# Kernel tuning notes

Measured on AMD Instinct MI355X. Metric: run time of the kernel, lower is better.

The kernel has to match this reference:

```python
import jax, jax.numpy as jnp
import numpy as np

B, S, D = 32, 577, 768
H, Dh = 12, 64  # num_attention_heads, attention_head_size = pruned_dim // heads


def setup_inputs() -> dict:
    key = jax.random.key(0)
    ks = jax.random.split(key, 7)
    s = 1.0 / np.sqrt(D)
    return {
        "hidden_states": jax.random.normal(ks[0], (B, S, D), dtype=jnp.float32),
        "Wq": jax.random.normal(ks[1], (D, H * Dh), dtype=jnp.float32) * s,
        "bq": jnp.zeros((H * Dh,), dtype=jnp.float32),
        "Wk": jax.random.normal(ks[2], (D, H * Dh), dtype=jnp.float32) * s,
        "bk": jnp.zeros((H * Dh,), dtype=jnp.float32),
        "Wv": jax.random.normal(ks[3], (D, H * Dh), dtype=jnp.float32) * s,
        "bv": jnp.zeros((H * Dh,), dtype=jnp.float32),
    }


def reference(hidden_states, Wq, bq, Wk, bk, Wv, bv):
    def heads(x):  # [B,S,H*Dh] -> [B,H,S,Dh]
        return x.reshape(B, S, H, Dh).transpose(0, 2, 1, 3)

    q = heads(hidden_states @ Wq + bq)
    k = heads(hidden_states @ Wk + bk)
    v = heads(hidden_states @ Wv + bv)

    scale = 1.0 / np.sqrt(Dh)
    scores = jnp.einsum("bhqd,bhkd->bhqk", q, k) * scale  # [B,H,S,S]
    probs = jax.nn.softmax(scores, axis=-1)  # dropout p=0.0 -> identity
    ctx = jnp.einsum("bhqk,bhkd->bhqd", probs, v)  # [B,H,S,Dh]
    ctx = ctx.transpose(0, 2, 1, 3).reshape(B, S, H * Dh)
    return ctx
```

## Files before the change

kernel.cpp:

```cpp
#include <hip/hip_runtime.h>

#define NB 32
#define SEQ 577
#define SP 640
#define DM 768
#define NH 12
#define DH 64
#define NC 10

typedef __attribute__((ext_vector_type(8))) short bf16x8;
typedef __attribute__((ext_vector_type(4))) short bf16x4;
typedef __attribute__((ext_vector_type(4))) float f32x4;
typedef __attribute__((ext_vector_type(2))) unsigned int u32x2;
typedef __attribute__((ext_vector_type(4))) unsigned int u32x4;
typedef unsigned short u16;

__device__ __forceinline__ u16 f2bf(float f) {
  unsigned int u = __builtin_bit_cast(unsigned int, f);
  u += 0x7fffu + ((u >> 16) & 1u);
  return (u16)(u >> 16);
}

__device__ __forceinline__ unsigned int pack_bf2(float a, float b) {
  unsigned int ua = __builtin_bit_cast(unsigned int, a) + 0x8000u;
  unsigned int ub = __builtin_bit_cast(unsigned int, b) + 0x8000u;
  return __builtin_amdgcn_perm(ub, ua, 0x07060302u);
}

__device__ __forceinline__ void g2l16(const void* g, void* lds) {
  __builtin_amdgcn_global_load_lds(
      (const __attribute__((address_space(1))) void*)g,
      (__attribute__((address_space(3))) void*)lds, 16, 0, 0);
}

__global__ void cvt_x_kernel(const float* __restrict__ X, u16* __restrict__ Xb, int n4) {
  int i = blockIdx.x * 256 + threadIdx.x;
  if (i >= n4) return;
  f32x4 v = *reinterpret_cast<const f32x4*>(X + (size_t)i * 4);
  u32x2 p;
  p[0] = (unsigned)f2bf(v[0]) | ((unsigned)f2bf(v[1]) << 16);
  p[1] = (unsigned)f2bf(v[2]) | ((unsigned)f2bf(v[3]) << 16);
  *reinterpret_cast<u32x2*>(Xb + (size_t)i * 4) = p;
}

__global__ __launch_bounds__(256)
void cvt_w_kernel(const float* __restrict__ Wq, const float* __restrict__ Wk,
                  const float* __restrict__ Wv, u16* __restrict__ Wt) {
  __shared__ u16 ld[64 * 72];
  const int m = blockIdx.z;
  const float* W = (m == 0) ? Wq : (m == 1) ? Wk : Wv;
  const int k0 = blockIdx.y * 64, n0 = blockIdx.x * 64;
  const int tid = threadIdx.x;
  const int kr = tid >> 4, c4 = tid & 15;
#pragma unroll
  for (int p = 0; p < 4; ++p) {
    const int k = p * 16 + kr;
    f32x4 v = *reinterpret_cast<const f32x4*>(&W[(size_t)(k0 + k) * DM + n0 + c4 * 4]);
#pragma unroll
    for (int e = 0; e < 4; ++e) ld[(c4 * 4 + e) * 72 + k] = f2bf(v[e]);
  }
  __syncthreads();
  u16* dst = Wt + (size_t)m * DM * DM;
#pragma unroll
  for (int p = 0; p < 2; ++p) {
    const int s = p * 256 + tid;
    const int n = s >> 3, ch = (s & 7) * 8;
    u32x4 w = *reinterpret_cast<const u32x4*>(&ld[n * 72 + ch]);
    *reinterpret_cast<u32x4*>(&dst[(size_t)(n0 + n) * DM + k0 + ch]) = w;
  }
}

__global__ __launch_bounds__(512, 2)
void qkv_gemm_kernel(const u16* __restrict__ Xb, const u16* __restrict__ Wt,
                     const float* __restrict__ bq, const float* __restrict__ bk,
                     const float* __restrict__ bv,
                     u16* __restrict__ Qw, u16* __restrict__ Kw, u16* __restrict__ Vw,
                     const int qkv) {
  __shared__ alignas(16) u16 sh[256 * 264];

  const int tid = threadIdx.x;
  const int lane = tid & 63;
  const int wid = tid >> 6;
  const int wm = wid >> 2, wn = wid & 3;
  const int l15 = lane & 15, lq = lane >> 4;

  const int flat = blockIdx.y * 80 + blockIdx.x;
  const int xcd = flat & 7;
  const int j8 = flat >> 3;
  const int xi = j8 / 3;
  const int nt = j8 - xi * 3;
  const int mt = xi * 8 + xcd;

  const u16* Wm = Wt + (size_t)qkv * DM * DM;
  const float* bias = (qkv == 0) ? bq : (qkv == 1) ? bk : bv;

  const u16* gA[2];
  const u16* gB[2];
#pragma unroll
  for (int s = 0; s < 2; ++s) {
    const int e = wid * 2 + s;
    int r = mt * 256 + e * 16 + l15;
    int br = r / SP;
    int tr = r - br * SP;
    if (tr >= SEQ) tr = SEQ - 1;
    gA[s] = Xb + (size_t)(br * SEQ + tr) * DM + lq * 8;
    gB[s] = Wm + (size_t)(nt * 256 + e * 16 + l15) * DM + lq * 8;
  }

  f32x4 acc[8][4];
#pragma unroll
  for (int i = 0; i < 8; ++i)
#pragma unroll
    for (int j = 0; j < 4; ++j)
#pragma unroll
      for (int r = 0; r < 4; ++r) acc[i][j][r] = 0.0f;

  auto stageA = [&](int buf, int kt) {
    g2l16(gA[0] + kt * 32, &sh[buf * 8192 + (wid * 2 + 0) * 512]);
    g2l16(gA[1] + kt * 32, &sh[buf * 8192 + (wid * 2 + 1) * 512]);
  };
  auto stageB = [&](int buf, int kt) {
    g2l16(gB[0] + kt * 32, &sh[32768 + buf * 8192 + (wid * 2 + 0) * 512]);
    g2l16(gB[1] + kt * 32, &sh[32768 + buf * 8192 + (wid * 2 + 1) * 512]);
  };

  stageA(0, 0); stageB(0, 0);
  stageA(1, 1); stageB(1, 1);
  stageA(2, 2); stageB(2, 2);
  asm volatile("s_waitcnt vmcnt(8)" ::: "memory");
  __builtin_amdgcn_s_barrier();

  const int NKT = DM / 32;
  for (int kt = 0; kt < NKT; ++kt) {
    const int buf = kt & 3;
    const int nbuf = (kt + 3) & 3;
    const bool more = (kt + 3 < NKT);
    bf16x8 a03[4], bf4[4], a47[4];

#pragma unroll
    for (int i = 0; i < 4; ++i)
      a03[i] = *reinterpret_cast<const bf16x8*>(&sh[buf * 8192 + ((wm * 8 + i) * 64 + lane) * 8]);
#pragma unroll
    for (int j = 0; j < 4; ++j)
      bf4[j] = *reinterpret_cast<const bf16x8*>(&sh[32768 + buf * 8192 + ((wn * 4 + j) * 64 + lane) * 8]);
    if (more) stageA(nbuf, kt + 3);
    __builtin_amdgcn_s_barrier();
    __builtin_amdgcn_s_setprio(1);
#pragma unroll
    for (int i = 0; i < 4; ++i)
#pragma unroll
      for (int j = 0; j < 4; ++j)
        acc[i][j] = __builtin_amdgcn_mfma_f32_16x16x32_bf16(a03[i], bf4[j], acc[i][j], 0, 0, 0);
    __builtin_amdgcn_s_setprio(0);
    __builtin_amdgcn_s_barrier();

#pragma unroll
    for (int i = 0; i < 4; ++i)
      a47[i] = *reinterpret_cast<const bf16x8*>(&sh[buf * 8192 + ((wm * 8 + 4 + i) * 64 + lane) * 8]);
    if (more) stageB(nbuf, kt + 3);
    if (kt <= NKT - 4) {
      asm volatile("s_waitcnt vmcnt(8)" ::: "memory");
    } else if (kt == NKT - 3) {
      asm volatile("s_waitcnt vmcnt(4)" ::: "memory");
    } else if (kt == NKT - 2) {
      asm volatile("s_waitcnt vmcnt(0)" ::: "memory");
    }
    __builtin_amdgcn_s_barrier();
    __builtin_amdgcn_s_setprio(1);
#pragma unroll
    for (int i = 0; i < 4; ++i)
#pragma unroll
      for (int j = 0; j < 4; ++j)
        acc[4 + i][j] = __builtin_amdgcn_mfma_f32_16x16x32_bf16(a47[i], bf4[j], acc[4 + i][j], 0, 0, 0);
    __builtin_amdgcn_s_setprio(0);
    __builtin_amdgcn_s_barrier();
  }

  const float sfold = 0.18033688011112042f;
#pragma unroll
  for (int j = 0; j < 4; ++j) {
    const int col = wn * 64 + j * 16 + l15;
    const float bb = bias[nt * 256 + col];
#pragma unroll
    for (int i = 0; i < 8; ++i) {
      const int row = wm * 128 + i * 16 + lq * 4;
      if (qkv == 2) {
        unsigned p0 = (unsigned)f2bf(acc[i][j][0] + bb) | ((unsigned)f2bf(acc[i][j][1] + bb) << 16);
        unsigned p1 = (unsigned)f2bf(acc[i][j][2] + bb) | ((unsigned)f2bf(acc[i][j][3] + bb) << 16);
        *reinterpret_cast<u32x2*>(&sh[col * 264 + row]) = u32x2{p0, p1};
      } else {
#pragma unroll
        for (int r = 0; r < 4; ++r) {
          float v = acc[i][j][r] + bb;
          if (qkv == 0) v *= sfold;
          sh[(row + r) * 264 + col] = f2bf(v);
        }
      }
    }
  }
  __builtin_amdgcn_s_barrier();

#pragma unroll
  for (int p = 0; p < 16; ++p) {
    const int slot = p * 512 + tid;
    const int rr = slot >> 5;
    const int cc = (slot & 31) * 8;
    u32x4 w = *reinterpret_cast<const u32x4*>(&sh[rr * 264 + cc]);
    if (qkv == 2) {
      const int gcol = nt * 256 + rr;
      const int h = gcol >> 6, d = gcol & 63;
      const int rg = mt * 256 + cc;
      const int br = rg / SP, tr = rg - br * SP;
      *reinterpret_cast<u32x4*>(&Vw[((size_t)(br * NH + h) * DH + d) * SP + tr]) = w;
    } else {
      const int rg = mt * 256 + rr;
      const int br = rg / SP, tr = rg - br * SP;
      const int gcol = nt * 256 + cc;
      const int h = gcol >> 6, d = gcol & 63;
      u16* dst = ((qkv == 0) ? Qw : Kw) + ((size_t)(br * NH + h) * SP + tr) * DH + d;
      *reinterpret_cast<u32x4*>(dst) = w;
    }
  }
}

#if __has_builtin(__builtin_amdgcn_mfma_f32_16x16x16bf16_1k)
#define MFMA16(a, b, c) __builtin_amdgcn_mfma_f32_16x16x16bf16_1k(a, b, c, 0, 0, 0)
#define HAVE_MFMA16 1
#elif __has_builtin(__builtin_amdgcn_mfma_f32_16x16x16_bf16)
#define MFMA16(a, b, c) __builtin_amdgcn_mfma_f32_16x16x16_bf16(a, b, c, 0, 0, 0)
#define HAVE_MFMA16 1
#else
#define HAVE_MFMA16 0
#endif

__global__ __launch_bounds__(256)
void attn_kernel(const u16* __restrict__ Qw, const u16* __restrict__ Kw,
                 const u16* __restrict__ Vw, float* __restrict__ out) {
  __shared__ alignas(16) u16 Kc[2][8 * 64 * 8];
  __shared__ alignas(16) u16 Vc[2][16 * 64 * 4];

  const int tid = threadIdx.x;
  const int lane = tid & 63;
  const int wid = tid >> 6;
  const int l15 = lane & 15, lq = lane >> 4;

  const int flat = blockIdx.y * 5 + blockIdx.x;
  const int w = (flat & 7) * 240 + (flat >> 3);
  const int qx = w % 5;
  const int bh = w / 5;
  const int b = bh / NH;
  const int h = bh - b * NH;
  const int q0 = qx * 128 + wid * 32;

  const u16* Qb = Qw + (size_t)bh * SP * DH;
  const u16* Kb = Kw + (size_t)bh * SP * DH;
  const u16* Vb = Vw + (size_t)bh * DH * SP;

  bf16x8 qf[2][2];
#pragma unroll
  for (int qt = 0; qt < 2; ++qt)
#pragma unroll
    for (int hf = 0; hf < 2; ++hf)
      qf[qt][hf] = *reinterpret_cast<const bf16x8*>(
          &Qb[(q0 + qt * 16 + l15) * DH + hf * 32 + lq * 8]);

  const u16* gK = Kb + (size_t)(wid * 16 + l15) * DH + lq * 8;
  const u16* gV = Vb + (size_t)(wid * 16 + l15) * SP + lq * 4;

  float mrow[2] = {-__builtin_inff(), -__builtin_inff()};
  float lrow[2] = {0.0f, 0.0f};
  f32x4 acc[2][4];
#pragma unroll
  for (int qt = 0; qt < 2; ++qt)
#pragma unroll
    for (int dt = 0; dt < 4; ++dt)
#pragma unroll
      for (int r = 0; r < 4; ++r) acc[qt][dt][r] = 0.0f;

  g2l16(gK, &Kc[0][(wid * 2 + 0) * 512]);
  g2l16(gK + 32, &Kc[0][(wid * 2 + 1) * 512]);
  {
    u32x2 v[4];
#pragma unroll
    for (int t = 0; t < 4; ++t)
      v[t] = *reinterpret_cast<const u32x2*>(gV + t * 16);
#pragma unroll
    for (int t = 0; t < 4; ++t)
      *reinterpret_cast<u32x2*>(&Vc[0][((wid * 4 + t) * 64 + lane) * 4]) = v[t];
  }
  __syncthreads();

  for (int c = 0; c < NC; ++c) {
    const int cur = c & 1;
    const int c0 = c * 64;
    u32x2 vn[4];
    if (c + 1 < NC) {
      const u16* gKn = gK + (size_t)(c0 + 64) * DH;
      g2l16(gKn, &Kc[cur ^ 1][(wid * 2 + 0) * 512]);
      g2l16(gKn + 32, &Kc[cur ^ 1][(wid * 2 + 1) * 512]);
#pragma unroll
      for (int t = 0; t < 4; ++t)
        vn[t] = *reinterpret_cast<const u32x2*>(gV + (c0 + 64) + t * 16);
    }

    f32x4 s[2][4];
    __builtin_amdgcn_s_setprio(1);
#pragma unroll
    for (int t = 0; t < 4; ++t) {
      bf16x8 kf0 = *reinterpret_cast<const bf16x8*>(&Kc[cur][((t * 2 + 0) * 64 + lane) * 8]);
      bf16x8 kf1 = *reinterpret_cast<const bf16x8*>(&Kc[cur][((t * 2 + 1) * 64 + lane) * 8]);
#pragma unroll
      for (int qt = 0; qt < 2; ++qt) {
        f32x4 z;
#pragma unroll
        for (int r = 0; r < 4; ++r) z[r] = 0.0f;
        z = __builtin_amdgcn_mfma_f32_16x16x32_bf16(kf0, qf[qt][0], z, 0, 0, 0);
        z = __builtin_amdgcn_mfma_f32_16x16x32_bf16(kf1, qf[qt][1], z, 0, 0, 0);
        s[qt][t] = z;
      }
    }
    __builtin_amdgcn_s_setprio(0);
    if (c0 + 64 > SEQ) {
#pragma unroll
      for (int qt = 0; qt < 2; ++qt)
#pragma unroll
        for (int t = 0; t < 4; ++t)
#pragma unroll
          for (int r = 0; r < 4; ++r) {
            int key = c0 + t * 16 + lq * 4 + r;
            s[qt][t][r] = (key < SEQ) ? s[qt][t][r] : -__builtin_inff();
          }
    }
    float alpha[2];
    unsigned int pku[2][4][2];
#pragma unroll
    for (int qt = 0; qt < 2; ++qt) {
      float mx = s[qt][0][0];
#pragma unroll
      for (int t = 0; t < 4; ++t)
#pragma unroll
        for (int r = 0; r < 4; ++r) mx = fmaxf(mx, s[qt][t][r]);
      mx = fmaxf(mx, __shfl_xor(mx, 16));
      mx = fmaxf(mx, __shfl_xor(mx, 32));
      float mn = fmaxf(mrow[qt], mx);
      alpha[qt] = __builtin_amdgcn_exp2f(mrow[qt] - mn);
      mrow[qt] = mn;
      float sm = 0.0f;
#pragma unroll
      for (int t = 0; t < 4; ++t) {
        float p0 = __builtin_amdgcn_exp2f(s[qt][t][0] - mn);
        float p1 = __builtin_amdgcn_exp2f(s[qt][t][1] - mn);
        float p2 = __builtin_amdgcn_exp2f(s[qt][t][2] - mn);
        float p3 = __builtin_amdgcn_exp2f(s[qt][t][3] - mn);
        sm += (p0 + p1) + (p2 + p3);
        pku[qt][t][0] = pack_bf2(p0, p1);
        pku[qt][t][1] = pack_bf2(p2, p3);
      }
      sm += __shfl_xor(sm, 16);
      sm += __shfl_xor(sm, 32);
      lrow[qt] = lrow[qt] * alpha[qt] + sm;
    }

#if HAVE_MFMA16
    __builtin_amdgcn_s_setprio(1);
#pragma unroll
    for (int dt = 0; dt < 4; ++dt) {
      bf16x4 vf[4];
#pragma unroll
      for (int t = 0; t < 4; ++t)
        vf[t] = *reinterpret_cast<const bf16x4*>(&Vc[cur][((dt * 4 + t) * 64 + lane) * 4]);
#pragma unroll
      for (int qt = 0; qt < 2; ++qt) {
        f32x4 a = acc[qt][dt];
#pragma unroll
        for (int r = 0; r < 4; ++r) a[r] *= alpha[qt];
#pragma unroll
        for (int t = 0; t < 4; ++t) {
          bf16x4 pf = __builtin_bit_cast(bf16x4, u32x2{pku[qt][t][0], pku[qt][t][1]});
          a = MFMA16(vf[t], pf, a);
        }
        acc[qt][dt] = a;
      }
    }
    __builtin_amdgcn_s_setprio(0);
#else
#pragma unroll
    for (int qt = 0; qt < 2; ++qt) {
      unsigned int bfrag[2][4];
#pragma unroll
      for (int hh = 0; hh < 2; ++hh)
#pragma unroll
        for (int w2 = 0; w2 < 4; ++w2) {
          int srcl = l15 + 16 * (2 * (lq & 1) + (w2 >> 1));
          unsigned int lo = (unsigned int)__shfl((int)pku[qt][2 * hh][w2 & 1], srcl);
          unsigned int hi = (unsigned int)__shfl((int)pku[qt][2 * hh + 1][w2 & 1], srcl);
          bfrag[hh][w2] = (lq < 2) ? lo : hi;
        }
#pragma unroll
      for (int dt = 0; dt < 4; ++dt) {
        f32x4 a = acc[qt][dt];
#pragma unroll
        for (int r = 0; r < 4; ++r) a[r] *= alpha[qt];
#pragma unroll
        for (int hh = 0; hh < 2; ++hh) {
          u32x2 w0 = *reinterpret_cast<const u32x2*>(&Vc[cur][((dt * 4 + 2 * hh) * 64 + lane) * 4]);
          u32x2 w1 = *reinterpret_cast<const u32x2*>(&Vc[cur][((dt * 4 + 2 * hh + 1) * 64 + lane) * 4]);
          u32x4 vw = {w0[0], w0[1], w1[0], w1[1]};
          u32x4 pw = {bfrag[hh][0], bfrag[hh][1], bfrag[hh][2], bfrag[hh][3]};
          a = __builtin_amdgcn_mfma_f32_16x16x32_bf16(
              __builtin_bit_cast(bf16x8, vw), __builtin_bit_cast(bf16x8, pw), a, 0, 0, 0);
        }
        acc[qt][dt] = a;
      }
    }
#endif

    if (c + 1 < NC) {
#pragma unroll
      for (int t = 0; t < 4; ++t)
        *reinterpret_cast<u32x2*>(&Vc[cur ^ 1][((wid * 4 + t) * 64 + lane) * 4]) = vn[t];
    }
    __syncthreads();
  }

#pragma unroll
  for (int qt = 0; qt < 2; ++qt) {
    int q = q0 + qt * 16 + l15;
    if (q < SEQ) {
      float rl = 1.0f / lrow[qt];
      float* orow = out + ((size_t)b * SEQ + q) * DM + h * DH;
#pragma unroll
      for (int dt = 0; dt < 4; ++dt) {
        f32x4 v = acc[qt][dt];
#pragma unroll
        for (int r = 0; r < 4; ++r) v[r] *= rl;
        *reinterpret_cast<f32x4*>(&orow[dt * 16 + lq * 4]) = v;
      }
    }
  }
}

extern "C" void kernel_launch(void* const* d_in, const int* in_sizes, int n_in,
                              void* d_out, int out_size, void* d_ws, size_t ws_size,
                              hipStream_t stream) {
  (void)in_sizes; (void)n_in; (void)out_size; (void)ws_size;
  const float* X  = (const float*)d_in[0];
  const float* Wq = (const float*)d_in[1];
  const float* bq = (const float*)d_in[2];
  const float* Wk = (const float*)d_in[3];
  const float* bk = (const float*)d_in[4];
  const float* Wv = (const float*)d_in[5];
  const float* bv = (const float*)d_in[6];
  float* out = (float*)d_out;

  char* ws = (char*)d_ws;
  u16* Xb = (u16*)ws;
  u16* Wt = (u16*)(ws + 28366848);
  u16* Qw = (u16*)(ws + 28366848 + 3538944);
  u16* Kw = Qw + (size_t)NB * NH * SP * DH;
  u16* Vw = Kw + (size_t)NB * NH * SP * DH;

  cvt_x_kernel<<<dim3(13848), 256, 0, stream>>>(X, Xb, 3545088);
  cvt_w_kernel<<<dim3(12, 12, 3), 256, 0, stream>>>(Wq, Wk, Wv, Wt);
  qkv_gemm_kernel<<<dim3(80, 3), 512, 0, stream>>>(Xb, Wt, bq, bk, bv, Qw, Kw, Vw, 0);
  qkv_gemm_kernel<<<dim3(80, 3), 512, 0, stream>>>(Xb, Wt, bq, bk, bv, Qw, Kw, Vw, 1);
  qkv_gemm_kernel<<<dim3(80, 3), 512, 0, stream>>>(Xb, Wt, bq, bk, bv, Qw, Kw, Vw, 2);
  attn_kernel<<<dim3(5, NB * NH), 256, 0, stream>>>(Qw, Kw, Vw, out);
}
```

Baseline: 307.1 us.

## Merge QKV GEMM launches and skip online-softmax rescale when max barely changes

The three per-projection QKV GEMM launches become one launch with a z dimension, and the block index is remapped so Q/K/V tiles share the XCD swizzle. This cuts launch gaps and tail underutilisation. In attention, the row max is found with a tree reduction, and when every lane's new max exceeds the running max by at most 8 (log2 domain) the old max is kept. That skips the alpha exp and the accumulator rescale, in the style of FA4 lazy rescaling, at the cost of exponentials up to 2^8 that must stay within bf16/fp32 range.

```diff
diff --git a/kernel.cpp b/kernel.cpp
--- a/kernel.cpp
+++ b/kernel.cpp
@@ -74,8 +74,7 @@
 void qkv_gemm_kernel(const u16* __restrict__ Xb, const u16* __restrict__ Wt,
                      const float* __restrict__ bq, const float* __restrict__ bk,
                      const float* __restrict__ bv,
-                     u16* __restrict__ Qw, u16* __restrict__ Kw, u16* __restrict__ Vw,
-                     const int qkv) {
+                     u16* __restrict__ Qw, u16* __restrict__ Kw, u16* __restrict__ Vw) {
   __shared__ alignas(16) u16 sh[256 * 264];
 
   const int tid = threadIdx.x;
@@ -84,12 +83,14 @@
   const int wm = wid >> 2, wn = wid & 3;
   const int l15 = lane & 15, lq = lane >> 4;
 
-  const int flat = blockIdx.y * 80 + blockIdx.x;
+  const int flat = (blockIdx.z * 3 + blockIdx.y) * 80 + blockIdx.x;
   const int xcd = flat & 7;
   const int j8 = flat >> 3;
-  const int xi = j8 / 3;
-  const int nt = j8 - xi * 3;
+  const int xi = j8 / 9;
+  const int yz = j8 - xi * 9;
   const int mt = xi * 8 + xcd;
+  const int nt = yz % 3;
+  const int qkv = yz / 3;
 
   const u16* Wm = Wt + (size_t)qkv * DM * DM;
   const float* bias = (qkv == 0) ? bq : (qkv == 1) ? bk : bv;
@@ -332,18 +333,21 @@
           }
     }
     float alpha[2];
+    bool skipq[2];
     unsigned int pku[2][4][2];
 #pragma unroll
     for (int qt = 0; qt < 2; ++qt) {
-      float mx = s[qt][0][0];
-#pragma unroll
-      for (int t = 0; t < 4; ++t)
-#pragma unroll
-        for (int r = 0; r < 4; ++r) mx = fmaxf(mx, s[qt][t][r]);
+      float t0 = fmaxf(fmaxf(fmaxf(s[qt][0][0], s[qt][0][1]), s[qt][0][2]), s[qt][0][3]);
+      float t1 = fmaxf(fmaxf(fmaxf(s[qt][1][0], s[qt][1][1]), s[qt][1][2]), s[qt][1][3]);
+      float t2 = fmaxf(fmaxf(fmaxf(s[qt][2][0], s[qt][2][1]), s[qt][2][2]), s[qt][2][3]);
+      float t3 = fmaxf(fmaxf(fmaxf(s[qt][3][0], s[qt][3][1]), s[qt][3][2]), s[qt][3][3]);
+      float mx = fmaxf(fmaxf(fmaxf(t0, t1), t2), t3);
       mx = fmaxf(mx, __shfl_xor(mx, 16));
       mx = fmaxf(mx, __shfl_xor(mx, 32));
-      float mn = fmaxf(mrow[qt], mx);
-      alpha[qt] = __builtin_amdgcn_exp2f(mrow[qt] - mn);
+      const bool sk = __all(mx - mrow[qt] <= 8.0f) != 0;
+      skipq[qt] = sk;
+      float mn = sk ? mrow[qt] : fmaxf(mrow[qt], mx);
+      alpha[qt] = sk ? 1.0f : __builtin_amdgcn_exp2f(mrow[qt] - mn);
       mrow[qt] = mn;
       float sm = 0.0f;
 #pragma unroll
@@ -358,7 +362,7 @@
       }
       sm += __shfl_xor(sm, 16);
       sm += __shfl_xor(sm, 32);
-      lrow[qt] = lrow[qt] * alpha[qt] + sm;
+      lrow[qt] = sk ? (lrow[qt] + sm) : (lrow[qt] * alpha[qt] + sm);
     }
 
 #if HAVE_MFMA16
@@ -372,8 +376,10 @@
 #pragma unroll
       for (int qt = 0; qt < 2; ++qt) {
         f32x4 a = acc[qt][dt];
-#pragma unroll
-        for (int r = 0; r < 4; ++r) a[r] *= alpha[qt];
+        if (!skipq[qt]) {
+#pragma unroll
+          for (int r = 0; r < 4; ++r) a[r] *= alpha[qt];
+        }
 #pragma unroll
         for (int t = 0; t < 4; ++t) {
           bf16x4 pf = __builtin_bit_cast(bf16x4, u32x2{pku[qt][t][0], pku[qt][t][1]});
@@ -399,8 +405,10 @@
 #pragma unroll
       for (int dt = 0; dt < 4; ++dt) {
         f32x4 a = acc[qt][dt];
-#pragma unroll
-        for (int r = 0; r < 4; ++r) a[r] *= alpha[qt];
+        if (!skipq[qt]) {
+#pragma unroll
+          for (int r = 0; r < 4; ++r) a[r] *= alpha[qt];
+        }
 #pragma unroll
         for (int hh = 0; hh < 2; ++hh) {
           u32x2 w0 = *reinterpret_cast<const u32x2*>(&Vc[cur][((dt * 4 + 2 * hh) * 64 + lane) * 4]);
@@ -462,8 +470,6 @@
 
   cvt_x_kernel<<<dim3(13848), 256, 0, stream>>>(X, Xb, 3545088);
   cvt_w_kernel<<<dim3(12, 12, 3), 256, 0, stream>>>(Wq, Wk, Wv, Wt);
-  qkv_gemm_kernel<<<dim3(80, 3), 512, 0, stream>>>(Xb, Wt, bq, bk, bv, Qw, Kw, Vw, 0);
-  qkv_gemm_kernel<<<dim3(80, 3), 512, 0, stream>>>(Xb, Wt, bq, bk, bv, Qw, Kw, Vw, 1);
-  qkv_gemm_kernel<<<dim3(80, 3), 512, 0, stream>>>(Xb, Wt, bq, bk, bv, Qw, Kw, Vw, 2);
+  qkv_gemm_kernel<<<dim3(80, 3, 3), 512, 0, stream>>>(Xb, Wt, bq, bk, bv, Qw, Kw, Vw);
   attn_kernel<<<dim3(5, NB * NH), 256, 0, stream>>>(Qw, Kw, Vw, out);
 }
```

After: 312.7 us. About the same (+1.8%).

## Merge Q/K/V GEMM launches into one grid and simplify K-loop barriers

Applied to the files above, without the earlier changes.

The three separate QKV GEMM launches become one launch with a z dimension, and the block index decode now derives the qkv selector alongside the row and column tiles. Before, the 240-block grids each had a partial last wave on the 256 CUs; one 720-block grid removes two launch gaps and lets the three GEMMs overlap. The main loop now loads all eight A fragments at once, issues both A and B stages together, and runs all MFMAs after a single barrier instead of two half-steps. That costs more VGPRs for fragments and less interleaving of memory and compute inside an iteration.

```diff
diff --git a/kernel.cpp b/kernel.cpp
--- a/kernel.cpp
+++ b/kernel.cpp
@@ -74,8 +74,7 @@
 void qkv_gemm_kernel(const u16* __restrict__ Xb, const u16* __restrict__ Wt,
                      const float* __restrict__ bq, const float* __restrict__ bk,
                      const float* __restrict__ bv,
-                     u16* __restrict__ Qw, u16* __restrict__ Kw, u16* __restrict__ Vw,
-                     const int qkv) {
+                     u16* __restrict__ Qw, u16* __restrict__ Kw, u16* __restrict__ Vw) {
   __shared__ alignas(16) u16 sh[256 * 264];
 
   const int tid = threadIdx.x;
@@ -84,12 +83,14 @@
   const int wm = wid >> 2, wn = wid & 3;
   const int l15 = lane & 15, lq = lane >> 4;
 
-  const int flat = blockIdx.y * 80 + blockIdx.x;
+  const int flat = (blockIdx.z * 3 + blockIdx.y) * 80 + blockIdx.x;
   const int xcd = flat & 7;
   const int j8 = flat >> 3;
-  const int xi = j8 / 3;
-  const int nt = j8 - xi * 3;
+  const int xi = j8 / 9;
+  const int yz = j8 - xi * 9;
   const int mt = xi * 8 + xcd;
+  const int nt = yz % 3;
+  const int qkv = yz / 3;
 
   const u16* Wm = Wt + (size_t)qkv * DM * DM;
   const float* bias = (qkv == 0) ? bq : (qkv == 1) ? bk : bv;
@@ -135,29 +136,17 @@
     const int buf = kt & 3;
     const int nbuf = (kt + 3) & 3;
     const bool more = (kt + 3 < NKT);
-    bf16x8 a03[4], bf4[4], a47[4];
-
-#pragma unroll
-    for (int i = 0; i < 4; ++i)
-      a03[i] = *reinterpret_cast<const bf16x8*>(&sh[buf * 8192 + ((wm * 8 + i) * 64 + lane) * 8]);
+    bf16x8 af[8], bf4[4];
+
+#pragma unroll
+    for (int i = 0; i < 8; ++i)
+      af[i] = *reinterpret_cast<const bf16x8*>(&sh[buf * 8192 + ((wm * 8 + i) * 64 + lane) * 8]);
 #pragma unroll
     for (int j = 0; j < 4; ++j)
       bf4[j] = *reinterpret_cast<const bf16x8*>(&sh[32768 + buf * 8192 + ((wn * 4 + j) * 64 + lane) * 8]);
-    if (more) stageA(nbuf, kt + 3);
-    __builtin_amdgcn_s_barrier();
-    __builtin_amdgcn_s_setprio(1);
-#pragma unroll
-    for (int i = 0; i < 4; ++i)
-#pragma unroll
-      for (int j = 0; j < 4; ++j)
-        acc[i][j] = __builtin_amdgcn_mfma_f32_16x16x32_bf16(a03[i], bf4[j], acc[i][j], 0, 0, 0);
-    __builtin_amdgcn_s_setprio(0);
-    __builtin_amdgcn_s_barrier();
-
-#pragma unroll
-    for (int i = 0; i < 4; ++i)
-      a47[i] = *reinterpret_cast<const bf16x8*>(&sh[buf * 8192 + ((wm * 8 + 4 + i) * 64 + lane) * 8]);
-    if (more) stageB(nbuf, kt + 3);
+
+    if (more) { stageA(nbuf, kt + 3); stageB(nbuf, kt + 3); }
+
     if (kt <= NKT - 4) {
       asm volatile("s_waitcnt vmcnt(8)" ::: "memory");
     } else if (kt == NKT - 3) {
@@ -166,12 +155,13 @@
       asm volatile("s_waitcnt vmcnt(0)" ::: "memory");
     }
     __builtin_amdgcn_s_barrier();
+
     __builtin_amdgcn_s_setprio(1);
 #pragma unroll
-    for (int i = 0; i < 4; ++i)
+    for (int i = 0; i < 8; ++i)
 #pragma unroll
       for (int j = 0; j < 4; ++j)
-        acc[4 + i][j] = __builtin_amdgcn_mfma_f32_16x16x32_bf16(a47[i], bf4[j], acc[4 + i][j], 0, 0, 0);
+        acc[i][j] = __builtin_amdgcn_mfma_f32_16x16x32_bf16(af[i], bf4[j], acc[i][j], 0, 0, 0);
     __builtin_amdgcn_s_setprio(0);
     __builtin_amdgcn_s_barrier();
   }
@@ -462,8 +452,6 @@
 
   cvt_x_kernel<<<dim3(13848), 256, 0, stream>>>(X, Xb, 3545088);
   cvt_w_kernel<<<dim3(12, 12, 3), 256, 0, stream>>>(Wq, Wk, Wv, Wt);
-  qkv_gemm_kernel<<<dim3(80, 3), 512, 0, stream>>>(Xb, Wt, bq, bk, bv, Qw, Kw, Vw, 0);
-  qkv_gemm_kernel<<<dim3(80, 3), 512, 0, stream>>>(Xb, Wt, bq, bk, bv, Qw, Kw, Vw, 1);
-  qkv_gemm_kernel<<<dim3(80, 3), 512, 0, stream>>>(Xb, Wt, bq, bk, bv, Qw, Kw, Vw, 2);
+  qkv_gemm_kernel<<<dim3(80, 3, 3), 512, 0, stream>>>(Xb, Wt, bq, bk, bv, Qw, Kw, Vw);
   attn_kernel<<<dim3(5, NB * NH), 256, 0, stream>>>(Qw, Kw, Vw, out);
 }
```

Result: no change. 302.6 us (-1.5%).
